# Kernel optimization log

Measured on AMD Instinct MI355X. Metric: run time of the kernel, lower is better.

Reference implementation:

```python
import jax, jax.numpy as jnp
import numpy as np

DIM = 768
HEADS = 12
HEAD_DIM = DIM // HEADS
MLP_DIM = 4 * DIM
EPS = 1e-5


def setup_inputs() -> dict:
    key = jax.random.key(0)
    ks = jax.random.split(key, 8)
    s = lambda fan_in: 1.0 / np.sqrt(fan_in)
    return {
        "x": jax.random.normal(ks[0], (2, 2048, DIM), dtype=jnp.float32),
        "ln1_w": jnp.ones((DIM,), jnp.float32),
        "ln1_b": jnp.zeros((DIM,), jnp.float32),
        # weights stored [in, out]
        "qkv_w": jax.random.normal(ks[1], (DIM, 3 * DIM), jnp.float32) * s(DIM),
        "qkv_b": jnp.zeros((3 * DIM,), jnp.float32),
        "proj_w": jax.random.normal(ks[2], (DIM, DIM), jnp.float32) * s(DIM),
        "proj_b": jnp.zeros((DIM,), jnp.float32),
        "ln2_w": jnp.ones((DIM,), jnp.float32),
        "ln2_b": jnp.zeros((DIM,), jnp.float32),
        "lin1_w": jax.random.normal(ks[3], (DIM, MLP_DIM), jnp.float32) * s(DIM),
        "lin1_b": jnp.zeros((MLP_DIM,), jnp.float32),
        "lin2_w": jax.random.normal(ks[4], (MLP_DIM, DIM), jnp.float32) * s(MLP_DIM),
        "lin2_b": jnp.zeros((DIM,), jnp.float32),
    }


def _layernorm(x, w, b):
    mu = jnp.mean(x, axis=-1, keepdims=True)
    var = jnp.mean(jnp.square(x - mu), axis=-1, keepdims=True)
    return (x - mu) * jax.lax.rsqrt(var + EPS) * w + b


def _attention(x, qkv_w, qkv_b, proj_w, proj_b):
    B, N, C = x.shape
    qkv = (x @ qkv_w + qkv_b).reshape(B, N, 3, HEADS, HEAD_DIM)
    q, k, v = qkv[:, :, 0], qkv[:, :, 1], qkv[:, :, 2]  # [B, N, H, Dh]
    scale = HEAD_DIM ** -0.5
    attn = jnp.einsum("bqhd,bkhd->bhqk", q, k) * scale  # full NxN scores
    attn = jax.nn.softmax(attn, axis=-1)
    out = jnp.einsum("bhqk,bkhd->bqhd", attn, v).reshape(B, N, C)
    return out @ proj_w + proj_b


def reference(x, ln1_w, ln1_b, qkv_w, qkv_b, proj_w, proj_b,
              ln2_w, ln2_b, lin1_w, lin1_b, lin2_w, lin2_b):
    x = x + _attention(_layernorm(x, ln1_w, ln1_b), qkv_w, qkv_b, proj_w, proj_b)
    h = _layernorm(x, ln2_w, ln2_b)
    h = jax.nn.gelu(h @ lin1_w + lin1_b, approximate=False) @ lin2_w + lin2_b
    return x + h
```

## Files before the change

### kernel.cpp

```cpp
#include <hip/hip_runtime.h>
#include <hip/hip_bf16.h>
#include <math.h>

#define DIM 768
#define NTOK 4096
#define SEQ 2048
#define HEADS 12
#define HD 64

using bf16x8 = __attribute__((ext_vector_type(8))) __bf16;
using bf16x4 = __attribute__((ext_vector_type(4))) __bf16;
using short4v = __attribute__((ext_vector_type(4))) short;
using f32x4  = __attribute__((ext_vector_type(4))) float;
typedef unsigned short u16;

__device__ inline u16 f2bf(float f) {
  union { float f; unsigned u; } v; v.f = f;
  unsigned r = v.u + 0x7fffu + ((v.u >> 16) & 1u);
  return (u16)(r >> 16);
}

__device__ inline void pk2bf(float a, float b, u16* o0, u16* o1) {
  union { __hip_bfloat162 h; u16 u[2]; } cv;
  cv.h = __float22bfloat162_rn(make_float2(a, b));
  *o0 = cv.u[0];
  *o1 = cv.u[1];
}

__device__ inline unsigned pku32(float a, float b) {
  union { __hip_bfloat162 h; unsigned u; } cv;
  cv.h = __float22bfloat162_rn(make_float2(a, b));
  return cv.u;
}

__device__ inline float gelu_t(float x) {
  float z = x * (1.5957691216f + 0.0713548162f * x * x);
  return x / (1.0f + __expf(-z));
}

__device__ inline void gl_lds16(const u16* g, u16* l) {
  __builtin_amdgcn_global_load_lds(
      (const __attribute__((address_space(1))) unsigned int*)g,
      (__attribute__((address_space(3))) unsigned int*)l, 16, 0, 0);
}

__global__ __launch_bounds__(256) void ln_kernel(const float* __restrict__ x,
                                                 const float* __restrict__ w,
                                                 const float* __restrict__ b,
                                                 u16* __restrict__ y) {
  int row = blockIdx.x;
  int t = threadIdx.x;
  const float* xr = x + (size_t)row * DIM;
  float v0 = xr[t], v1 = xr[t + 256], v2 = xr[t + 512];
  float s = v0 + v1 + v2;
  float q = v0 * v0 + v1 * v1 + v2 * v2;
  for (int o = 32; o > 0; o >>= 1) {
    s += __shfl_down(s, o, 64);
    q += __shfl_down(q, o, 64);
  }
  __shared__ float ws_[4], wq_[4], mb[2];
  int wid = t >> 6;
  if ((t & 63) == 0) { ws_[wid] = s; wq_[wid] = q; }
  __syncthreads();
  if (t == 0) {
    float S = ws_[0] + ws_[1] + ws_[2] + ws_[3];
    float Q = wq_[0] + wq_[1] + wq_[2] + wq_[3];
    float mean = S * (1.0f / DIM);
    float var = Q * (1.0f / DIM) - mean * mean;
    mb[0] = mean;
    mb[1] = rsqrtf(var + 1e-5f);
  }
  __syncthreads();
  float mean = mb[0], rstd = mb[1];
  u16* yr = y + (size_t)row * DIM;
  yr[t]       = f2bf((v0 - mean) * rstd * w[t]       + b[t]);
  yr[t + 256] = f2bf((v1 - mean) * rstd * w[t + 256] + b[t + 256]);
  yr[t + 512] = f2bf((v2 - mean) * rstd * w[t + 512] + b[t + 512]);
}

__global__ __launch_bounds__(256) void redln_kernel(
    const float* __restrict__ P0, const float* __restrict__ P1,
    const float* __restrict__ bias, const float* __restrict__ res,
    float* __restrict__ x2, const float* __restrict__ lnw,
    const float* __restrict__ lnb, u16* __restrict__ y) {
  int row = blockIdx.x;
  int t = threadIdx.x;
  size_t off = (size_t)row * DIM;
  float v[3];
#pragma unroll
  for (int k = 0; k < 3; ++k) {
    int c = t + k * 256;
    v[k] = P0[off + c] + P1[off + c] + bias[c] + res[off + c];
    x2[off + c] = v[k];
  }
  float s = v[0] + v[1] + v[2];
  float q = v[0] * v[0] + v[1] * v[1] + v[2] * v[2];
  for (int o = 32; o > 0; o >>= 1) {
    s += __shfl_down(s, o, 64);
    q += __shfl_down(q, o, 64);
  }
  __shared__ float ws_[4], wq_[4], mb[2];
  int wid = t >> 6;
  if ((t & 63) == 0) { ws_[wid] = s; wq_[wid] = q; }
  __syncthreads();
  if (t == 0) {
    float S = ws_[0] + ws_[1] + ws_[2] + ws_[3];
    float Q = wq_[0] + wq_[1] + wq_[2] + wq_[3];
    float mean = S * (1.0f / DIM);
    float var = Q * (1.0f / DIM) - mean * mean;
    mb[0] = mean;
    mb[1] = rsqrtf(var + 1e-5f);
  }
  __syncthreads();
  float mean = mb[0], rstd = mb[1];
#pragma unroll
  for (int k = 0; k < 3; ++k) {
    int c = t + k * 256;
    y[off + c] = f2bf((v[k] - mean) * rstd * lnw[c] + lnb[c]);
  }
}

__global__ __launch_bounds__(256) void wcvt_all(
    const float* __restrict__ W0, const float* __restrict__ W1,
    const float* __restrict__ W2, const float* __restrict__ W3,
    u16* __restrict__ T0, u16* __restrict__ T1,
    u16* __restrict__ T2, u16* __restrict__ T3) {
  int id = blockIdx.x;
  const float* W; u16* Wt; int K, N, local;
  if (id < 1728)      { W = W0; Wt = T0; K = 768;  N = 2304; local = id; }
  else if (id < 2304) { W = W1; Wt = T1; K = 768;  N = 768;  local = id - 1728; }
  else if (id < 4608) { W = W2; Wt = T2; K = 768;  N = 3072; local = id - 2304; }
  else                { W = W3; Wt = T3; K = 3072; N = 768;  local = id - 4608; }
  int ntiles = N / 32;
  int n0 = (local % ntiles) * 32, k0 = (local / ntiles) * 32;
  __shared__ float tile[32][33];
  int tid = threadIdx.x;
  int c = tid & 31, r8 = tid >> 5;
#pragma unroll
  for (int p = 0; p < 4; ++p) {
    int k = r8 + p * 8;
    tile[k][c] = W[(size_t)(k0 + k) * N + n0 + c];
  }
  __syncthreads();
#pragma unroll
  for (int p = 0; p < 4; ++p) {
    int n = r8 + p * 8;
    Wt[(size_t)(n0 + n) * K + k0 + c] = f2bf(tile[c][n]);
  }
}

__global__ __launch_bounds__(256) void vtr_kernel(const u16* __restrict__ qkvB,
                                                  u16* __restrict__ vT) {
  __shared__ u16 tile[32][33];
  int v0 = blockIdx.x * 32, j0 = blockIdx.y * 32, b = blockIdx.z;
  int tid = threadIdx.x;
  int c = tid & 31, r8 = tid >> 5;
#pragma unroll
  for (int p = 0; p < 4; ++p) {
    int r = r8 + p * 8;
    tile[r][c] = qkvB[((size_t)(b * SEQ + j0 + r)) * 2304 + 1536 + v0 + c];
  }
  __syncthreads();
#pragma unroll
  for (int p = 0; p < 4; ++p) {
    int r = r8 + p * 8;
    vT[((size_t)(b * 768 + v0 + r)) * SEQ + j0 + c] = tile[c][r];
  }
}

__global__ __launch_bounds__(256) void bgemm_kernel(
    const u16* __restrict__ A, const u16* __restrict__ Bt,
    const float* __restrict__ bias, u16* __restrict__ Cb,
    int M, int N, int K, int act) {
  __shared__ __align__(16) u16 Asl[128 * 64];
  __shared__ __align__(16) u16 Bsl[128 * 64];
  int tid = threadIdx.x;
  int lane = tid & 63, wave = tid >> 6;
  int wm = wave >> 1, wn = wave & 1;
  int bm = blockIdx.y * 128, bn = blockIdx.x * 128;
  int l15 = lane & 15, quad = lane >> 4;
  int sm8 = tid >> 3;
  int kgx = (tid & 7) ^ (sm8 & 7);

  f32x4 acc[4][4] = {};
  const u16* Ap = A + (size_t)(bm + sm8) * K + kgx * 8;
  const u16* Bp = Bt + (size_t)(bn + sm8) * K + kgx * 8;
  u16* Al = &Asl[(wave * 8) * 64];
  u16* Bl = &Bsl[(wave * 8) * 64];
  int xr = l15 & 7;

  for (int k0 = 0; k0 < K; k0 += 64) {
#pragma unroll
    for (int p = 0; p < 4; ++p)
      gl_lds16(Ap + (size_t)(p * 32) * K + k0, Al + p * 32 * 64);
#pragma unroll
    for (int p = 0; p < 4; ++p)
      gl_lds16(Bp + (size_t)(p * 32) * K + k0, Bl + p * 32 * 64);
    __syncthreads();
#pragma unroll
    for (int ks = 0; ks < 2; ++ks) {
      int pu = ((ks << 2) + quad) ^ xr;
      bf16x8 af[4], bfr[4];
#pragma unroll
      for (int i = 0; i < 4; ++i) {
        af[i]  = *(const bf16x8*)&Asl[(wm * 64 + i * 16 + l15) * 64 + pu * 8];
        bfr[i] = *(const bf16x8*)&Bsl[(wn * 64 + i * 16 + l15) * 64 + pu * 8];
      }
#pragma unroll
      for (int i = 0; i < 4; ++i)
#pragma unroll
        for (int j = 0; j < 4; ++j)
          acc[i][j] = __builtin_amdgcn_mfma_f32_16x16x32_bf16(af[i], bfr[j], acc[i][j], 0, 0, 0);
    }
    __syncthreads();
  }

#pragma unroll
  for (int i = 0; i < 4; ++i) {
#pragma unroll
    for (int j = 0; j < 4; ++j) {
      int n = bn + wn * 64 + j * 16 + l15;
      float bv = bias[n];
      float val[4];
#pragma unroll
      for (int r = 0; r < 4; ++r) {
        float v = acc[i][j][r] + bv;
        val[r] = act ? gelu_t(v) : v;
      }
      u16 c0, c1, c2, c3;
      pk2bf(val[0], val[1], &c0, &c1);
      pk2bf(val[2], val[3], &c2, &c3);
      size_t mbase = (size_t)(bm + wm * 64 + i * 16 + quad * 4) * N + n;
      Cb[mbase]         = c0;
      Cb[mbase + N]     = c1;
      Cb[mbase + 2 * N] = c2;
      Cb[mbase + 3 * N] = c3;
    }
  }
}

__global__ __launch_bounds__(256) void bgemm_splitk(
    const u16* __restrict__ A, const u16* __restrict__ Bt,
    float* __restrict__ P0, float* __restrict__ P1,
    int M, int N, int K) {
  __shared__ __align__(16) u16 Asl[128 * 64];
  __shared__ __align__(16) u16 Bsl[64 * 64];
  int tid = threadIdx.x;
  int lane = tid & 63, wave = tid >> 6;
  int wm = wave >> 1, wn = wave & 1;
  int bm = blockIdx.y * 128, bn = blockIdx.x * 64;
  int l15 = lane & 15, quad = lane >> 4;
  int sm8 = tid >> 3;
  int kgx = (tid & 7) ^ (sm8 & 7);
  int half = K >> 1;
  int kbeg = blockIdx.z * half;

  f32x4 acc[4][2] = {};
  const u16* Ap = A + (size_t)(bm + sm8) * K + kbeg + kgx * 8;
  const u16* Bp = Bt + (size_t)(bn + sm8) * K + kbeg + kgx * 8;
  u16* Al = &Asl[(wave * 8) * 64];
  u16* Bl = &Bsl[(wave * 8) * 64];
  int xr = l15 & 7;

  for (int k0 = 0; k0 < half; k0 += 64) {
#pragma unroll
    for (int p = 0; p < 4; ++p)
      gl_lds16(Ap + (size_t)(p * 32) * K + k0, Al + p * 32 * 64);
#pragma unroll
    for (int p = 0; p < 2; ++p)
      gl_lds16(Bp + (size_t)(p * 32) * K + k0, Bl + p * 32 * 64);
    __syncthreads();
#pragma unroll
    for (int ks = 0; ks < 2; ++ks) {
      int pu = ((ks << 2) + quad) ^ xr;
      bf16x8 af[4], bfr[2];
#pragma unroll
      for (int i = 0; i < 4; ++i)
        af[i] = *(const bf16x8*)&Asl[(wm * 64 + i * 16 + l15) * 64 + pu * 8];
#pragma unroll
      for (int j = 0; j < 2; ++j)
        bfr[j] = *(const bf16x8*)&Bsl[(wn * 32 + j * 16 + l15) * 64 + pu * 8];
#pragma unroll
      for (int i = 0; i < 4; ++i)
#pragma unroll
        for (int j = 0; j < 2; ++j)
          acc[i][j] = __builtin_amdgcn_mfma_f32_16x16x32_bf16(af[i], bfr[j], acc[i][j], 0, 0, 0);
    }
    __syncthreads();
  }

  float* P = blockIdx.z ? P1 : P0;
#pragma unroll
  for (int i = 0; i < 4; ++i) {
#pragma unroll
    for (int j = 0; j < 2; ++j) {
      int n = bn + wn * 32 + j * 16 + l15;
#pragma unroll
      for (int r = 0; r < 4; ++r) {
        int m = bm + wm * 64 + i * 16 + quad * 4 + r;
        P[(size_t)m * N + n] = acc[i][j][r];
      }
    }
  }
}

__global__ __launch_bounds__(256) void red_kernel(
    const float* P0, const float* __restrict__ P1,
    const float* __restrict__ bias, const float* __restrict__ res,
    float* O, int Ncols) {
  int i = blockIdx.x * 256 + threadIdx.x;
  float4 a = ((const float4*)P0)[i];
  float4 b = ((const float4*)P1)[i];
  float4 r = ((const float4*)res)[i];
  int col = (i * 4) % Ncols;
  float4 bi = *(const float4*)&bias[col];
  float4 o;
  o.x = a.x + b.x + r.x + bi.x;
  o.y = a.y + b.y + r.y + bi.y;
  o.z = a.z + b.z + r.z + bi.z;
  o.w = a.w + b.w + r.w + bi.w;
  ((float4*)O)[i] = o;
}

#define LDP 68
__global__ __launch_bounds__(256, 3) void attn_kernel(const u16* __restrict__ qkv,
                                                      const u16* __restrict__ vT,
                                                      u16* __restrict__ out) {
  __shared__ __align__(16) char arena[40960];
  u16* Qsp = (u16*)arena;
  u16* Ksp = (u16*)(arena + 8192);
  u16* Vsp = (u16*)(arena + 24576);

  int tid = threadIdx.x;
  int lane = tid & 63, wave = tid >> 6;
  int l15 = lane & 15, quad = lane >> 4;
  int qt = blockIdx.x * 64;
  int h = blockIdx.y, b = blockIdx.z;
  size_t base = (size_t)b * SEQ;
  int srow = lane >> 3;
  int sux = (lane & 7) ^ (srow & 7);
  int r0 = wave * 16;
  const u16* qbase = qkv + (base + qt) * 2304 + h * HD;
  const u16* kbase = qkv + base * 2304 + 768 + h * HD;
  const u16* vbase = vT + ((size_t)(b * HEADS + h) * HD) * SEQ;

  gl_lds16(qbase + (size_t)(r0 + srow) * 2304 + sux * 8, Qsp + r0 * 64);
  gl_lds16(qbase + (size_t)(r0 + 8 + srow) * 2304 + sux * 8, Qsp + (r0 + 8) * 64);
  gl_lds16(kbase + (size_t)(r0 + srow) * 2304 + sux * 8, Ksp + r0 * 64);
  gl_lds16(kbase + (size_t)(r0 + 8 + srow) * 2304 + sux * 8, Ksp + (r0 + 8) * 64);
  gl_lds16(vbase + (size_t)(r0 + srow) * SEQ + sux * 8, Vsp + r0 * 64);
  gl_lds16(vbase + (size_t)(r0 + 8 + srow) * SEQ + sux * 8, Vsp + (r0 + 8) * 64);
  __syncthreads();

  int xr = l15 & 7;
  bf16x8 qf[4][2];
#pragma unroll
  for (int g = 0; g < 4; ++g)
#pragma unroll
    for (int s = 0; s < 2; ++s)
      qf[g][s] = *(const bf16x8*)&Qsp[(g * 16 + l15) * 64 + ((s * 4 + quad) ^ xr) * 8];

  int koff0 = (wave * 16 + l15) * 64 + ((quad ^ xr)) * 8;
  int koff1 = (wave * 16 + l15) * 64 + (((4 + quad) ^ xr)) * 8;
  int voff[4];
#pragma unroll
  for (int dg = 0; dg < 4; ++dg)
    voff[dg] = (dg * 16 + l15) * 64 + (((2 * wave + (quad >> 1)) ^ xr)) * 8 + (quad & 1) * 4;

  f32x4 oT[4][4] = {};
  float lsum[4] = {0.f, 0.f, 0.f, 0.f};
  const float KEXP = 0.18033688011112042f;

  for (int t = 0; t < 32; ++t) {
    int buf = t & 1;
    if (t < 31) {
      size_t kt1 = (size_t)(t + 1) * 64;
      u16* Kd = Ksp + (buf ^ 1) * 4096;
      u16* Vd = Vsp + (buf ^ 1) * 4096;
      gl_lds16(kbase + (kt1 + r0 + srow) * 2304 + sux * 8, Kd + r0 * 64);
      gl_lds16(kbase + (kt1 + r0 + 8 + srow) * 2304 + sux * 8, Kd + (r0 + 8) * 64);
      gl_lds16(vbase + (size_t)(r0 + srow) * SEQ + kt1 + sux * 8, Vd + r0 * 64);
      gl_lds16(vbase + (size_t)(r0 + 8 + srow) * SEQ + kt1 + sux * 8, Vd + (r0 + 8) * 64);
    }
    const u16* Kb = Ksp + buf * 4096;
    const u16* Vb = Vsp + buf * 4096;

    f32x4 sT[4] = {};
    __builtin_amdgcn_s_setprio(1);
    {
      bf16x8 ak = *(const bf16x8*)&Kb[koff0];
#pragma unroll
      for (int g = 0; g < 4; ++g)
        sT[g] = __builtin_amdgcn_mfma_f32_16x16x32_bf16(ak, qf[g][0], sT[g], 0, 0, 0);
      bf16x8 ak1 = *(const bf16x8*)&Kb[koff1];
#pragma unroll
      for (int g = 0; g < 4; ++g)
        sT[g] = __builtin_amdgcn_mfma_f32_16x16x32_bf16(ak1, qf[g][1], sT[g], 0, 0, 0);
    }
    __builtin_amdgcn_s_setprio(0);

    short4v pb[4];
#pragma unroll
    for (int g = 0; g < 4; ++g) {
      float p0 = __builtin_amdgcn_exp2f(sT[g][0] * KEXP);
      float p1 = __builtin_amdgcn_exp2f(sT[g][1] * KEXP);
      float p2 = __builtin_amdgcn_exp2f(sT[g][2] * KEXP);
      float p3 = __builtin_amdgcn_exp2f(sT[g][3] * KEXP);
      lsum[g] += (p0 + p1) + (p2 + p3);
      union { unsigned u[2]; short4v s; } cv;
      cv.u[0] = pku32(p0, p1);
      cv.u[1] = pku32(p2, p3);
      pb[g] = cv.s;
    }

    short4v av[4];
#pragma unroll
    for (int dg = 0; dg < 4; ++dg)
      av[dg] = *(const short4v*)&Vb[voff[dg]];
    __builtin_amdgcn_s_setprio(1);
#pragma unroll
    for (int dg = 0; dg < 4; ++dg)
#pragma unroll
      for (int g = 0; g < 4; ++g)
        oT[dg][g] = __builtin_amdgcn_mfma_f32_16x16x16bf16_1k(av[dg], pb[g], oT[dg][g], 0, 0, 0);
    __builtin_amdgcn_s_setprio(0);
    __syncthreads();
  }

#pragma unroll
  for (int g = 0; g < 4; ++g) {
    lsum[g] += __shfl_xor(lsum[g], 16, 64);
    lsum[g] += __shfl_xor(lsum[g], 32, 64);
  }
  float* LDSw = (float*)arena;
  float* lsd  = (float*)(arena + 17408);
  if (lane < 16) {
#pragma unroll
    for (int g = 0; g < 4; ++g) lsd[wave * 64 + g * 16 + lane] = lsum[g];
  }
  float linv = 0.f;
#pragma unroll
  for (int dg = 0; dg < 4; ++dg) {
#pragma unroll
    for (int g = 0; g < 4; ++g)
#pragma unroll
      for (int r = 0; r < 4; ++r)
        LDSw[wave * (16 * LDP) + (quad * 4 + r) * LDP + g * 16 + l15] = oT[dg][g][r];
    __syncthreads();
    if (dg == 0) {
      float L = lsd[wave * 16 + l15] + lsd[64 + wave * 16 + l15] +
                lsd[128 + wave * 16 + l15] + lsd[192 + wave * 16 + l15];
      linv = 1.0f / L;
    }
    float sv[4];
#pragma unroll
    for (int i = 0; i < 4; ++i) {
      int dloc = quad * 4 + i;
      float a = LDSw[dloc * LDP + wave * 16 + l15] +
                LDSw[1 * (16 * LDP) + dloc * LDP + wave * 16 + l15] +
                LDSw[2 * (16 * LDP) + dloc * LDP + wave * 16 + l15] +
                LDSw[3 * (16 * LDP) + dloc * LDP + wave * 16 + l15];
      sv[i] = a * linv;
    }
    size_t addr = (base + qt + wave * 16 + l15) * DIM + h * HD + dg * 16 + quad * 4;
    uint2 pk;
    pk.x = pku32(sv[0], sv[1]);
    pk.y = pku32(sv[2], sv[3]);
    *(uint2*)&out[addr] = pk;
    __syncthreads();
  }
}

extern "C" void kernel_launch(void* const* d_in, const int* in_sizes, int n_in,
                              void* d_out, int out_size, void* d_ws, size_t ws_size,
                              hipStream_t stream) {
  const float* x     = (const float*)d_in[0];
  const float* ln1w  = (const float*)d_in[1];
  const float* ln1b  = (const float*)d_in[2];
  const float* qkvw  = (const float*)d_in[3];
  const float* qkvbi = (const float*)d_in[4];
  const float* projw = (const float*)d_in[5];
  const float* projb = (const float*)d_in[6];
  const float* ln2w  = (const float*)d_in[7];
  const float* ln2b  = (const float*)d_in[8];
  const float* l1w   = (const float*)d_in[9];
  const float* l1b   = (const float*)d_in[10];
  const float* l2w   = (const float*)d_in[11];
  const float* l2b   = (const float*)d_in[12];
  float* out = (float*)d_out;

  char* w = (char*)d_ws;
  u16*   h     = (u16*)w;   w += (size_t)NTOK * DIM * 2;
  u16*   qkvB  = (u16*)w;
  u16*   mid   = (u16*)w;   w += (size_t)NTOK * 3072 * 2;
  u16*   attnb = (u16*)w;   w += (size_t)NTOK * DIM * 2;
  float* x2    = (float*)w; w += (size_t)NTOK * DIM * 4;
  u16*   vTb   = (u16*)w;   w += (size_t)NTOK * DIM * 2;
  u16*   qkvwt = (u16*)w;   w += (size_t)DIM * 2304 * 2;
  u16*   projwt= (u16*)w;   w += (size_t)DIM * DIM * 2;
  u16*   l1wt  = (u16*)w;   w += (size_t)DIM * 3072 * 2;
  u16*   l2wt  = (u16*)w;   w += (size_t)3072 * DIM * 2;
  float* Pbuf  = (float*)w; w += (size_t)NTOK * DIM * 4;

  wcvt_all<<<6912, 256, 0, stream>>>(qkvw, projw, l1w, l2w,
                                     qkvwt, projwt, l1wt, l2wt);

  ln_kernel<<<NTOK, 256, 0, stream>>>(x, ln1w, ln1b, h);
  bgemm_kernel<<<dim3(2304 / 128, NTOK / 128), 256, 0, stream>>>(
      h, qkvwt, qkvbi, qkvB, NTOK, 2304, DIM, 0);
  vtr_kernel<<<dim3(768 / 32, SEQ / 32, 2), 256, 0, stream>>>(qkvB, vTb);
  attn_kernel<<<dim3(SEQ / 64, HEADS, 2), 256, 0, stream>>>(qkvB, vTb, attnb);

  bgemm_splitk<<<dim3(DIM / 64, NTOK / 128, 2), 256, 0, stream>>>(
      attnb, projwt, x2, Pbuf, NTOK, DIM, DIM);
  redln_kernel<<<NTOK, 256, 0, stream>>>(x2, Pbuf, projb, x, x2, ln2w, ln2b, h);

  bgemm_kernel<<<dim3(3072 / 128, NTOK / 128), 256, 0, stream>>>(
      h, l1wt, l1b, mid, NTOK, 3072, DIM, 1);

  bgemm_splitk<<<dim3(DIM / 64, NTOK / 128, 2), 256, 0, stream>>>(
      mid, l2wt, out, Pbuf, NTOK, DIM, 3072);
  red_kernel<<<NTOK * DIM / 1024, 256, 0, stream>>>(out, Pbuf, l2b, x2, out, DIM);
}
```

Baseline: 278.8 us.

## Fold softmax scale into QKV GEMM, compute row sums via MFMA, deepen K/V prefetch

Three changes to the attention path. The QKV GEMM epilogue now premultiplies Q by the softmax scale times log2(e), which removes a multiply per score in the attention loop. The per-row exp sum is computed with an extra MFMA against a ones vector instead of VALU adds and end-of-loop shuffles. The K/V loads are restructured to prefetch two tiles ahead with explicit vmcnt waits and split barriers, so global loads overlap more compute. In exchange, Q is rounded to bf16 after scaling and each iteration issues four extra MFMAs.

```diff
diff --git a/kernel.cpp b/kernel.cpp
--- a/kernel.cpp
+++ b/kernel.cpp
@@ -13,6 +13,8 @@
 using short4v = __attribute__((ext_vector_type(4))) short;
 using f32x4  = __attribute__((ext_vector_type(4))) float;
 typedef unsigned short u16;
+
+#define KEXPF 0.18033688011112042f
 
 __device__ inline u16 f2bf(float f) {
   union { float f; unsigned u; } v; v.f = f;
@@ -171,7 +173,7 @@
 __global__ __launch_bounds__(256) void bgemm_kernel(
     const u16* __restrict__ A, const u16* __restrict__ Bt,
     const float* __restrict__ bias, u16* __restrict__ Cb,
-    int M, int N, int K, int act) {
+    int M, int N, int K, int act, int scaleq) {
   __shared__ __align__(16) u16 Asl[128 * 64];
   __shared__ __align__(16) u16 Bsl[128 * 64];
   int tid = threadIdx.x;
@@ -221,10 +223,11 @@
     for (int j = 0; j < 4; ++j) {
       int n = bn + wn * 64 + j * 16 + l15;
       float bv = bias[n];
+      float cs = (scaleq && n < 768) ? KEXPF : 1.0f;
       float val[4];
 #pragma unroll
       for (int r = 0; r < 4; ++r) {
-        float v = acc[i][j][r] + bv;
+        float v = (acc[i][j][r] + bv) * cs;
         val[r] = act ? gelu_t(v) : v;
       }
       u16 c0, c1, c2, c3;
@@ -360,6 +363,11 @@
     for (int s = 0; s < 2; ++s)
       qf[g][s] = *(const bf16x8*)&Qsp[(g * 16 + l15) * 64 + ((s * 4 + quad) ^ xr) * 8];
 
+  gl_lds16(kbase + (size_t)(64 + r0 + srow) * 2304 + sux * 8, Ksp + 4096 + r0 * 64);
+  gl_lds16(kbase + (size_t)(64 + r0 + 8 + srow) * 2304 + sux * 8, Ksp + 4096 + (r0 + 8) * 64);
+  gl_lds16(vbase + (size_t)(r0 + srow) * SEQ + 64 + sux * 8, Vsp + 4096 + r0 * 64);
+  gl_lds16(vbase + (size_t)(r0 + 8 + srow) * SEQ + 64 + sux * 8, Vsp + 4096 + (r0 + 8) * 64);
+
   int koff0 = (wave * 16 + l15) * 64 + ((quad ^ xr)) * 8;
   int koff1 = (wave * 16 + l15) * 64 + (((4 + quad) ^ xr)) * 8;
   int voff[4];
@@ -368,20 +376,11 @@
     voff[dg] = (dg * 16 + l15) * 64 + (((2 * wave + (quad >> 1)) ^ xr)) * 8 + (quad & 1) * 4;
 
   f32x4 oT[4][4] = {};
-  float lsum[4] = {0.f, 0.f, 0.f, 0.f};
-  const float KEXP = 0.18033688011112042f;
+  f32x4 oT1[4] = {};
+  const short4v ONES = {(short)0x3F80, (short)0x3F80, (short)0x3F80, (short)0x3F80};
+  int buf = 0;
 
   for (int t = 0; t < 32; ++t) {
-    int buf = t & 1;
-    if (t < 31) {
-      size_t kt1 = (size_t)(t + 1) * 64;
-      u16* Kd = Ksp + (buf ^ 1) * 4096;
-      u16* Vd = Vsp + (buf ^ 1) * 4096;
-      gl_lds16(kbase + (kt1 + r0 + srow) * 2304 + sux * 8, Kd + r0 * 64);
-      gl_lds16(kbase + (kt1 + r0 + 8 + srow) * 2304 + sux * 8, Kd + (r0 + 8) * 64);
-      gl_lds16(vbase + (size_t)(r0 + srow) * SEQ + kt1 + sux * 8, Vd + r0 * 64);
-      gl_lds16(vbase + (size_t)(r0 + 8 + srow) * SEQ + kt1 + sux * 8, Vd + (r0 + 8) * 64);
-    }
     const u16* Kb = Ksp + buf * 4096;
     const u16* Vb = Vsp + buf * 4096;
 
@@ -402,11 +401,10 @@
     short4v pb[4];
 #pragma unroll
     for (int g = 0; g < 4; ++g) {
-      float p0 = __builtin_amdgcn_exp2f(sT[g][0] * KEXP);
-      float p1 = __builtin_amdgcn_exp2f(sT[g][1] * KEXP);
-      float p2 = __builtin_amdgcn_exp2f(sT[g][2] * KEXP);
-      float p3 = __builtin_amdgcn_exp2f(sT[g][3] * KEXP);
-      lsum[g] += (p0 + p1) + (p2 + p3);
+      float p0 = __builtin_amdgcn_exp2f(sT[g][0]);
+      float p1 = __builtin_amdgcn_exp2f(sT[g][1]);
+      float p2 = __builtin_amdgcn_exp2f(sT[g][2]);
+      float p3 = __builtin_amdgcn_exp2f(sT[g][3]);
       union { unsigned u[2]; short4v s; } cv;
       cv.u[0] = pku32(p0, p1);
       cv.u[1] = pku32(p2, p3);
@@ -423,20 +421,37 @@
 #pragma unroll
       for (int g = 0; g < 4; ++g)
         oT[dg][g] = __builtin_amdgcn_mfma_f32_16x16x16bf16_1k(av[dg], pb[g], oT[dg][g], 0, 0, 0);
+#pragma unroll
+    for (int g = 0; g < 4; ++g)
+      oT1[g] = __builtin_amdgcn_mfma_f32_16x16x16bf16_1k(ONES, pb[g], oT1[g], 0, 0, 0);
     __builtin_amdgcn_s_setprio(0);
-    __syncthreads();
-  }
-
-#pragma unroll
-  for (int g = 0; g < 4; ++g) {
-    lsum[g] += __shfl_xor(lsum[g], 16, 64);
-    lsum[g] += __shfl_xor(lsum[g], 32, 64);
-  }
+
+    __builtin_amdgcn_sched_barrier(0);
+    __builtin_amdgcn_s_barrier();
+    __builtin_amdgcn_sched_barrier(0);
+    if (t < 30) {
+      size_t kt2 = (size_t)(t + 2) * 64;
+      u16* Kd = Ksp + buf * 4096;
+      u16* Vd = Vsp + buf * 4096;
+      gl_lds16(kbase + (kt2 + r0 + srow) * 2304 + sux * 8, Kd + r0 * 64);
+      gl_lds16(kbase + (kt2 + r0 + 8 + srow) * 2304 + sux * 8, Kd + (r0 + 8) * 64);
+      gl_lds16(vbase + (size_t)(r0 + srow) * SEQ + kt2 + sux * 8, Vd + r0 * 64);
+      gl_lds16(vbase + (size_t)(r0 + 8 + srow) * SEQ + kt2 + sux * 8, Vd + (r0 + 8) * 64);
+      asm volatile("s_waitcnt vmcnt(4)" ::: "memory");
+    } else {
+      asm volatile("s_waitcnt vmcnt(0)" ::: "memory");
+    }
+    __builtin_amdgcn_sched_barrier(0);
+    __builtin_amdgcn_s_barrier();
+    __builtin_amdgcn_sched_barrier(0);
+    buf ^= 1;
+  }
+
   float* LDSw = (float*)arena;
   float* lsd  = (float*)(arena + 17408);
   if (lane < 16) {
 #pragma unroll
-    for (int g = 0; g < 4; ++g) lsd[wave * 64 + g * 16 + lane] = lsum[g];
+    for (int g = 0; g < 4; ++g) lsd[wave * 64 + g * 16 + lane] = oT1[g][0];
   }
   float linv = 0.f;
 #pragma unroll
@@ -507,7 +522,7 @@
 
   ln_kernel<<<NTOK, 256, 0, stream>>>(x, ln1w, ln1b, h);
   bgemm_kernel<<<dim3(2304 / 128, NTOK / 128), 256, 0, stream>>>(
-      h, qkvwt, qkvbi, qkvB, NTOK, 2304, DIM, 0);
+      h, qkvwt, qkvbi, qkvB, NTOK, 2304, DIM, 0, 1);
   vtr_kernel<<<dim3(768 / 32, SEQ / 32, 2), 256, 0, stream>>>(qkvB, vTb);
   attn_kernel<<<dim3(SEQ / 64, HEADS, 2), 256, 0, stream>>>(qkvB, vTb, attnb);
 
@@ -516,7 +531,7 @@
   redln_kernel<<<NTOK, 256, 0, stream>>>(x2, Pbuf, projb, x, x2, ln2w, ln2b, h);
 
   bgemm_kernel<<<dim3(3072 / 128, NTOK / 128), 256, 0, stream>>>(
-      h, l1wt, l1b, mid, NTOK, 3072, DIM, 1);
+      h, l1wt, l1b, mid, NTOK, 3072, DIM, 1, 0);
 
   bgemm_splitk<<<dim3(DIM / 64, NTOK / 128, 2), 256, 0, stream>>>(
       mid, l2wt, out, Pbuf, NTOK, DIM, 3072);
```

New measurement: 279.6 us. No clear change (+0.3%).
